# Kernel optimization log

Measured on AMD Instinct MI355X. Metric: run time of the kernel, lower is better.

## Reference

```python
import jax, jax.numpy as jnp
import numpy as np

N = 128       # HiPPO order
BATCH = 2
L = 2048      # max_length / sequence length
GBT_ALPHA = 0.5
STEP = 1.0


def _legs_transition(n_order):
    """HiPPO-LegS transition matrices A (N,N), B (N,1) as in TransMatrix(measure='legs')."""
    q = np.arange(n_order, dtype=np.float64)
    col, row = np.meshgrid(q, q)
    r = 2 * q + 1
    M = -(np.where(row >= col, r, 0.0) - np.diag(q))   # lower-tri + diag
    T = np.sqrt(2 * q + 1)
    A = (T[:, None] * M) / T[None, :]                  # T @ M @ inv(T)
    B = T[:, None]
    return A.astype(np.float32), B.astype(np.float32)


def setup_inputs() -> dict:
    key = jax.random.key(0)
    f = jax.random.normal(key, (BATCH, L, 1), dtype=jnp.float32)
    A_np, B_np = _legs_transition(N)
    return {
        "f": f,
        "A": jnp.asarray(A_np),
        "B": jnp.asarray(B_np),
        "C": jnp.ones((N, 1), dtype=jnp.float32),
        "D": jnp.zeros((1,), dtype=jnp.float32),
    }


def _discretize(A, B, step, alpha):
    """Generalized bilinear transform (alpha=0.5 -> bilinear)."""
    I = jnp.eye(A.shape[0], dtype=A.dtype)
    ss = 1.0 / step
    p1 = I - ss * alpha * A
    Ad = jnp.linalg.solve(p1, I + ss * (1.0 - alpha) * A)
    Bd = jnp.linalg.solve(p1, ss * B)
    return Ad, Bd


def reference(f, A, B, C, D):
    """HiPPO lti recurrence (verbose=False): returns (c_final, y_seq).
    c_final: (batch, 1, N); y_seq: (batch, L, N, N)."""
    n = A.shape[0]
    Ad, Bd = _discretize(A, B, STEP, GBT_ALPHA)          # (N,N), (N,1)
    c0 = jnp.zeros((f.shape[0], 1, n), dtype=f.dtype)     # init_state default
    f_t_first = jnp.swapaxes(f, 0, 1)                     # (L, batch, 1)

    def step(c, f_t):
        # c: (batch, 1, N), f_t: (batch, 1)
        c_new = c @ Ad.T + Bd.T * f_t[:, :, None]         # (batch, 1, N)
        # faithful to source: y_k = C @ c_k + D * f_k  ->  outer product (N,N)
        y = jnp.einsum('nm,bmk->bnk', C, c_new) + (D * f_t)[:, :, None]
        return c_new, y

    c_fin, ys = jax.lax.scan(step, c0, f_t_first)         # ys: (L, batch, N, N)
    ys = jnp.swapaxes(ys, 0, 1)                           # (batch, L, N, N)
    return c_fin, ys
```

## Files before the change

### kernel.cpp

```cpp
#include <hip/hip_runtime.h>
#include <math.h>

#define NSTATE 128
#define LSEQ   2048
#define NBATCH 2

typedef float f32x4 __attribute__((ext_vector_type(4)));

#define WS_AD   0
#define WS_BD   16384
#define WS_MB0  16512
#define WS_V    49280

__global__ void k_init(float* __restrict__ Ad, float* __restrict__ Bd,
                       float* __restrict__ V) {
    __shared__ double u[128], invd[128];
    int j = threadIdx.x;
    if (j < 128) { u[j] = sqrt(2.0 * j + 1.0); invd[j] = 1.0 / (1.0 + 0.5 * (j + 1)); }
    __syncthreads();
    if (j > 128) return;
    double S = 0.0;
    double uj = (j < 128) ? u[j] : 0.0;
    for (int i = 0; i < 128; ++i) {
        double ui = u[i];
        double b;
        if (j == 128)      b = ui;
        else if (i < j)    b = 0.0;
        else if (i == j)   b = 1.0 - 0.5 * (j + 1);
        else               b = -0.5 * ui * uj;
        double x = (b - 0.5 * ui * S) * invd[i];
        S += ui * x;
        if (j == 128) { Bd[i] = (float)x; V[i] = (float)x; }
        else Ad[i * 128 + j] = (float)x;
    }
}

__device__ __forceinline__ void chain_run(const float4 a[8], float4 vr[8],
                                          float* __restrict__ vb,
                                          int n, int h, int steps,
                                          float* __restrict__ Vst, int vstride,
                                          float* __restrict__ Mst) {
    for (int s = 1; s <= steps; ++s) {
        float s0 = 0.f, s1 = 0.f, s2 = 0.f, s3 = 0.f;
        #pragma unroll
        for (int q = 0; q < 8; ++q) {
            s0 = fmaf(a[q].x, vr[q].x, s0);
            s1 = fmaf(a[q].y, vr[q].y, s1);
            s2 = fmaf(a[q].z, vr[q].z, s2);
            s3 = fmaf(a[q].w, vr[q].w, s3);
        }
        float p = (s0 + s1) + (s2 + s3);
        p += __shfl_xor(p, 1);
        p += __shfl_xor(p, 2);
        float* cur = vb + (s & 1) * 144;
        if (h == 0) {
            cur[36 * (n >> 5) + (n & 31)] = p;
            if (Vst) Vst[s * vstride + n] = p;
            if (Mst && s == steps) Mst[n * 128] = p;
        }
        __syncthreads();
        const float4* vv = (const float4*)(cur + 36 * h);
        #pragma unroll
        for (int q = 0; q < 8; ++q) vr[q] = vv[q];
    }
}

__global__ __launch_bounds__(512) void k_pow(const float* __restrict__ Ad,
                                             const float* __restrict__ Bd,
                                             float* __restrict__ V,
                                             float* __restrict__ M) {
    int blk = blockIdx.x, tid = threadIdx.x;
    int n = tid >> 2, h = tid & 3;
    __shared__ float vb[2 * 144];
    float4 a[8];
    const float4* Ar = (const float4*)(Ad + n * 128 + 32 * h);
    #pragma unroll
    for (int q = 0; q < 8; ++q) a[q] = Ar[q];
    float4 vr[8];
    if (blk == 128) {
        const float4* Bv = (const float4*)(Bd + 32 * h);
        #pragma unroll
        for (int q = 0; q < 8; ++q) vr[q] = Bv[q];
        chain_run(a, vr, vb, n, h, 31, V, 128, nullptr);
    } else {
        #pragma unroll
        for (int q = 0; q < 8; ++q) {
            vr[q].x = (32 * h + 4 * q + 0 == blk) ? 1.f : 0.f;
            vr[q].y = (32 * h + 4 * q + 1 == blk) ? 1.f : 0.f;
            vr[q].z = (32 * h + 4 * q + 2 == blk) ? 1.f : 0.f;
            vr[q].w = (32 * h + 4 * q + 3 == blk) ? 1.f : 0.f;
        }
        chain_run(a, vr, vb, n, h, 32, nullptr, 0, M + blk);
    }
}

__global__ __launch_bounds__(512) void k_starts(const float* __restrict__ M,
                                                const float* __restrict__ Bd,
                                                float* __restrict__ V) {
    int tid = threadIdx.x;
    int n = tid >> 2, h = tid & 3;
    __shared__ float vb[2 * 144];
    float4 a[8];
    const float4* Ar = (const float4*)(M + n * 128 + 32 * h);
    #pragma unroll
    for (int q = 0; q < 8; ++q) a[q] = Ar[q];
    float4 vr[8];
    const float4* Bv = (const float4*)(Bd + 32 * h);
    #pragma unroll
    for (int q = 0; q < 8; ++q) vr[q] = Bv[q];
    chain_run(a, vr, vb, n, h, 63, V, 32 * 128, nullptr);
}

__global__ __launch_bounds__(512) void k_tails(const float* __restrict__ Ad,
                                               float* __restrict__ V) {
    int c = blockIdx.x + 1, tid = threadIdx.x;
    int n = tid >> 2, h = tid & 3;
    __shared__ float vb[2 * 144];
    float4 a[8];
    const float4* Ar = (const float4*)(Ad + n * 128 + 32 * h);
    #pragma unroll
    for (int q = 0; q < 8; ++q) a[q] = Ar[q];
    float4 vr[8];
    float* Vrow = V + (size_t)c * 32 * 128;
    const float4* Sv = (const float4*)(Vrow + 32 * h);
    #pragma unroll
    for (int q = 0; q < 8; ++q) vr[q] = Sv[q];
    chain_run(a, vr, vb, n, h, 31, Vrow, 128, nullptr);
}

__global__ __launch_bounds__(512) void k_convwrite(const float* __restrict__ f,
                                                   const float* __restrict__ V,
                                                   float* __restrict__ out) {
    int b = blockIdx.x, tile = blockIdx.y;
    int t0 = tile * 8;
    int Dtot = t0 + 8;
    __shared__ float fL[2080];
    __shared__ float red[4][8][128];
    int tid = threadIdx.x;
    if (tid < 15) fL[tid] = 0.f;
    for (int x = tid; x < Dtot; x += 512) fL[15 + x] = f[b * LSEQ + x];
    __syncthreads();

    int k = tid & 127, h = tid >> 7;
    float acc[8];
    #pragma unroll
    for (int i = 0; i < 8; ++i) acc[i] = 0.f;

    int nblk = (Dtot + 15) >> 4;
    for (int ib = h; ib < nblk; ib += 4) {
        int dbase = ib << 4;
        int foff = t0 - dbase;
        float F[24];
        const f32x4* fv = (const f32x4*)(fL + foff);
        #pragma unroll
        for (int q = 0; q < 6; ++q) {
            f32x4 t4 = fv[q];
            F[4 * q] = t4.x; F[4 * q + 1] = t4.y; F[4 * q + 2] = t4.z; F[4 * q + 3] = t4.w;
        }
        const float* Vp = V + (size_t)dbase * 128 + k;
        #pragma unroll
        for (int dd = 0; dd < 16; ++dd) {
            float w = Vp[dd * 128];
            #pragma unroll
            for (int i = 0; i < 8; ++i)
                acc[i] = fmaf(w, F[15 + i - dd], acc[i]);
        }
    }

    #pragma unroll
    for (int i = 0; i < 8; ++i) red[h][i][k] = acc[i];
    __syncthreads();
    if (tid < 128) {
        #pragma unroll
        for (int i = 0; i < 8; ++i) {
            float s = red[0][i][tid] + red[1][i][tid] + red[2][i][tid] + red[3][i][tid];
            red[0][i][tid] = s;
        }
    }
    __syncthreads();

    const f32x4* outv = (const f32x4*)&red[0][0][0];
    int k32 = tid & 31, r0 = tid >> 5;
    float* ysb = out + 256 + ((size_t)(b * LSEQ + t0)) * 16384;
    #pragma unroll
    for (int t = 0; t < 8; ++t) {
        f32x4 v = outv[t * 32 + k32];
        float* yst = ysb + (size_t)t * 16384 + k32 * 4;
        #pragma unroll
        for (int p = 0; p < 8; ++p) {
            int n = p * 16 + r0;
            __builtin_nontemporal_store(v, (f32x4*)(yst + n * 128));
        }
    }
    if (tile == 255 && tid < 32)
        *(f32x4*)(out + b * 128 + tid * 4) = outv[7 * 32 + tid];
}

extern "C" void kernel_launch(void* const* d_in, const int* in_sizes, int n_in,
                              void* d_out, int out_size, void* d_ws, size_t ws_size,
                              hipStream_t stream) {
    const float* f = (const float*)d_in[0];
    float* ws   = (float*)d_ws;
    float* Ad   = ws + WS_AD;
    float* Bd   = ws + WS_BD;
    float* M32  = ws + WS_MB0;
    float* V    = ws + WS_V;
    float* out  = (float*)d_out;

    k_init  <<<1,   256, 0, stream>>>(Ad, Bd, V);
    k_pow   <<<129, 512, 0, stream>>>(Ad, Bd, V, M32);
    k_starts<<<1,   512, 0, stream>>>(M32, Bd, V);
    k_tails <<<63,  512, 0, stream>>>(Ad, V);
    dim3 cw(2, 256);
    k_convwrite<<<cw, 512, 0, stream>>>(f, V, out);
}
```

Measured before the change: 340.4 us.

## Fold discretization into power kernels and compute chunk starts per block

Removes the separate init and serial start-state kernels. Each block of the power and tails kernels now solves for Ad/Bd itself in shared memory, using a padded stride. Each tails block then derives its own chunk start by applying M=Ad^32 c times to Bd before propagating with Ad. This cuts two kernel launches and the single-block 63-step serial start chain, at the cost of redundant double-precision solves in every block and longer chains for high-index blocks.

```diff
diff --git a/kernel.cpp b/kernel.cpp
--- a/kernel.cpp
+++ b/kernel.cpp
@@ -7,18 +7,16 @@
 
 typedef float f32x4 __attribute__((ext_vector_type(4)));
 
-#define WS_AD   0
-#define WS_BD   16384
-#define WS_MB0  16512
-#define WS_V    49280
-
-__global__ void k_init(float* __restrict__ Ad, float* __restrict__ Bd,
-                       float* __restrict__ V) {
-    __shared__ double u[128], invd[128];
-    int j = threadIdx.x;
-    if (j < 128) { u[j] = sqrt(2.0 * j + 1.0); invd[j] = 1.0 / (1.0 + 0.5 * (j + 1)); }
-    __syncthreads();
-    if (j > 128) return;
+#define WS_MB0  0
+#define WS_V    16384
+
+__device__ __forceinline__ void solve_AdBd(float* __restrict__ Ads,
+                                           float* __restrict__ Bds,
+                                           const double* __restrict__ u,
+                                           const double* __restrict__ invd,
+                                           int tid) {
+    if (tid > 128) return;
+    int j = tid;
     double S = 0.0;
     double uj = (j < 128) ? u[j] : 0.0;
     for (int i = 0; i < 128; ++i) {
@@ -30,8 +28,8 @@
         else               b = -0.5 * ui * uj;
         double x = (b - 0.5 * ui * S) * invd[i];
         S += ui * x;
-        if (j == 128) { Bd[i] = (float)x; V[i] = (float)x; }
-        else Ad[i * 128 + j] = (float)x;
+        if (j == 128) Bds[i] = (float)x;
+        else          Ads[i * 132 + j] = (float)x;
     }
 }
 
@@ -65,20 +63,27 @@
     }
 }
 
-__global__ __launch_bounds__(512) void k_pow(const float* __restrict__ Ad,
-                                             const float* __restrict__ Bd,
-                                             float* __restrict__ V,
-                                             float* __restrict__ M) {
-    int blk = blockIdx.x, tid = threadIdx.x;
+__global__ __launch_bounds__(512) void k_pow2(float* __restrict__ M,
+                                              float* __restrict__ V) {
+    __shared__ float Ads[128 * 132];
+    __shared__ float Bds[132];
+    __shared__ double u[128], invd[128];
+    __shared__ float vb[2 * 144];
+    int tid = threadIdx.x, blk = blockIdx.x;
+    if (tid < 128) { u[tid] = sqrt(2.0 * tid + 1.0); invd[tid] = 1.0 / (1.0 + 0.5 * (tid + 1)); }
+    __syncthreads();
+    solve_AdBd(Ads, Bds, u, invd, tid);
+    __syncthreads();
+
     int n = tid >> 2, h = tid & 3;
-    __shared__ float vb[2 * 144];
     float4 a[8];
-    const float4* Ar = (const float4*)(Ad + n * 128 + 32 * h);
+    const float4* Ar = (const float4*)(Ads + n * 132 + 32 * h);
     #pragma unroll
     for (int q = 0; q < 8; ++q) a[q] = Ar[q];
     float4 vr[8];
     if (blk == 128) {
-        const float4* Bv = (const float4*)(Bd + 32 * h);
+        if (tid < 128) V[tid] = Bds[tid];
+        const float4* Bv = (const float4*)(Bds + 32 * h);
         #pragma unroll
         for (int q = 0; q < 8; ++q) vr[q] = Bv[q];
         chain_run(a, vr, vb, n, h, 31, V, 128, nullptr);
@@ -94,38 +99,38 @@
     }
 }
 
-__global__ __launch_bounds__(512) void k_starts(const float* __restrict__ M,
-                                                const float* __restrict__ Bd,
+__global__ __launch_bounds__(512) void k_tails2(const float* __restrict__ M,
                                                 float* __restrict__ V) {
-    int tid = threadIdx.x;
+    __shared__ float Ads[128 * 132];
+    __shared__ float Bds[132];
+    __shared__ double u[128], invd[128];
+    __shared__ float vb[2 * 144];
+    int tid = threadIdx.x, c = blockIdx.x + 1;
+    if (tid < 128) { u[tid] = sqrt(2.0 * tid + 1.0); invd[tid] = 1.0 / (1.0 + 0.5 * (tid + 1)); }
+    __syncthreads();
+    solve_AdBd(Ads, Bds, u, invd, tid);
+    __syncthreads();
+
     int n = tid >> 2, h = tid & 3;
-    __shared__ float vb[2 * 144];
-    float4 a[8];
-    const float4* Ar = (const float4*)(M + n * 128 + 32 * h);
-    #pragma unroll
-    for (int q = 0; q < 8; ++q) a[q] = Ar[q];
-    float4 vr[8];
-    const float4* Bv = (const float4*)(Bd + 32 * h);
+    float4 am[8], aa[8], vr[8];
+    const float4* Mr = (const float4*)(M + n * 128 + 32 * h);
+    #pragma unroll
+    for (int q = 0; q < 8; ++q) am[q] = Mr[q];
+    const float4* Ar = (const float4*)(Ads + n * 132 + 32 * h);
+    #pragma unroll
+    for (int q = 0; q < 8; ++q) aa[q] = Ar[q];
+    const float4* Bv = (const float4*)(Bds + 32 * h);
     #pragma unroll
     for (int q = 0; q < 8; ++q) vr[q] = Bv[q];
-    chain_run(a, vr, vb, n, h, 63, V, 32 * 128, nullptr);
-}
-
-__global__ __launch_bounds__(512) void k_tails(const float* __restrict__ Ad,
-                                               float* __restrict__ V) {
-    int c = blockIdx.x + 1, tid = threadIdx.x;
-    int n = tid >> 2, h = tid & 3;
-    __shared__ float vb[2 * 144];
-    float4 a[8];
-    const float4* Ar = (const float4*)(Ad + n * 128 + 32 * h);
-    #pragma unroll
-    for (int q = 0; q < 8; ++q) a[q] = Ar[q];
-    float4 vr[8];
+
+    chain_run(am, vr, vb, n, h, c, nullptr, 0, nullptr);
     float* Vrow = V + (size_t)c * 32 * 128;
-    const float4* Sv = (const float4*)(Vrow + 32 * h);
-    #pragma unroll
-    for (int q = 0; q < 8; ++q) vr[q] = Sv[q];
-    chain_run(a, vr, vb, n, h, 31, Vrow, 128, nullptr);
+    if (n == 0) {
+        #pragma unroll
+        for (int q = 0; q < 8; ++q) ((float4*)Vrow)[8 * h + q] = vr[q];
+    }
+    __syncthreads();
+    chain_run(aa, vr, vb, n, h, 31, Vrow, 128, nullptr);
 }
 
 __global__ __launch_bounds__(512) void k_convwrite(const float* __restrict__ f,
@@ -201,16 +206,12 @@
                               hipStream_t stream) {
     const float* f = (const float*)d_in[0];
     float* ws   = (float*)d_ws;
-    float* Ad   = ws + WS_AD;
-    float* Bd   = ws + WS_BD;
     float* M32  = ws + WS_MB0;
     float* V    = ws + WS_V;
     float* out  = (float*)d_out;
 
-    k_init  <<<1,   256, 0, stream>>>(Ad, Bd, V);
-    k_pow   <<<129, 512, 0, stream>>>(Ad, Bd, V, M32);
-    k_starts<<<1,   512, 0, stream>>>(M32, Bd, V);
-    k_tails <<<63,  512, 0, stream>>>(Ad, V);
+    k_pow2  <<<129, 512, 0, stream>>>(M32, V);
+    k_tails2<<<63,  512, 0, stream>>>(M32, V);
     dim3 cw(2, 256);
     k_convwrite<<<cw, 512, 0, stream>>>(f, V, out);
 }
```

Result: no change. 342.0 us (+0.5%).
